# Performance work log

Measured on AMD Instinct MI355X. Metric: run time of the kernel, lower is better.

The kernel has to match this reference:

```python
import jax, jax.numpy as jnp
import numpy as np

B = 2
NUM_EDGES = 50000          # line-graph nodes per sample
N = B * NUM_EDGES          # total nodes in batched graph
E = 400000                 # connectivity edges (before self-loops)
F_IN = 16                  # num_edge_features
TDIM = 64                  # time_embedding_dim
H, C = 4, 32               # heads, hidden_channels
HC = H * C                 # 128
NL_EXTRA = 3               # num_layers - 1
NCLASS = 2
THETA = 1.0
MAX_TIME = 1000.0
NEG_SLOPE = 0.2            # GATv2 leaky_relu slope (PyG default)

def _p(key, shape, s=0.05):
    return jax.random.normal(key, shape, dtype=jnp.float32) * s

def setup_inputs() -> dict:
    key = jax.random.key(0)
    ks = jax.random.split(key, 16)
    return {
        "x": jax.random.normal(ks[0], (N, F_IN), dtype=jnp.float32),
        "edge_index": jax.random.randint(ks[1], (2, E), 0, N, dtype=jnp.int32),
        "t": jax.random.randint(ks[2], (B,), 0, 1000, dtype=jnp.int32),
        "tW0": _p(ks[3], (TDIM, TDIM)), "tb0": jnp.zeros((TDIM,), jnp.float32),
        "tW1": _p(ks[4], (TDIM, TDIM)), "tb1": jnp.zeros((TDIM,), jnp.float32),
        "c0_Wl": _p(ks[5], (F_IN + TDIM, HC)), "c0_bl": jnp.zeros((HC,), jnp.float32),
        "c0_Wr": _p(ks[6], (F_IN + TDIM, HC)), "c0_br": jnp.zeros((HC,), jnp.float32),
        "c0_att": _p(ks[7], (H, C)), "c0_bias": jnp.zeros((HC,), jnp.float32),
        "r0_W": _p(ks[8], (F_IN + TDIM, HC)), "r0_b": jnp.zeros((HC,), jnp.float32),
        "cWl": _p(ks[9], (NL_EXTRA, HC, HC)),
        "cWr": _p(ks[10], (NL_EXTRA, HC, HC)),
        "catt": _p(ks[11], (NL_EXTRA, H, C)),
        "rW": _p(ks[12], (NL_EXTRA, HC, HC)), "rb": jnp.zeros((NL_EXTRA, HC), jnp.float32),
        "fdW": _p(ks[13], (HC, C)), "fdb": jnp.zeros((C,), jnp.float32),
        "acW": _p(ks[14], (C, NCLASS)), "acb": jnp.zeros((NCLASS,), jnp.float32),
    }

def _timestep_embedding(t):
    # Fairseq-style sinusoidal embedding, matches get_timestep_embedding
    ts = t.astype(jnp.float32) * (1000.0 / MAX_TIME)
    half = TDIM // 2
    freqs = jnp.exp(jnp.arange(half, dtype=jnp.float32) * (-jnp.log(10000.0) / (half - 1)))
    ang = ts[:, None] * freqs[None, :]
    return jnp.concatenate([jnp.sin(ang), jnp.cos(ang)], axis=1)  # [B, TDIM]

def _gatv2(x, Wl, bl, Wr, br, att, src, dst):
    # PyG GATv2Conv, concat=True, add_self_loops already in src/dst
    xl = x @ Wl
    xr = x @ Wr
    if bl is not None:
        xl = xl + bl
    if br is not None:
        xr = xr + br
    xl = xl.reshape(N, H, C)
    xr = xr.reshape(N, H, C)
    g = jax.nn.leaky_relu(xl[src] + xr[dst], NEG_SLOPE)          # [Etot, H, C]
    e = jnp.einsum('ehc,hc->eh', g, att)                          # [Etot, H]
    m = jax.ops.segment_max(e, dst, num_segments=N)
    ex = jnp.exp(e - m[dst])
    denom = jax.ops.segment_sum(ex, dst, num_segments=N)
    alpha = ex / denom[dst]
    out = jax.ops.segment_sum(alpha[:, :, None] * xl[src], dst, num_segments=N)
    return out.reshape(N, HC)

def reference(x, edge_index, t, tW0, tb0, tW1, tb1, c0_Wl, c0_bl, c0_Wr, c0_br,
              c0_att, c0_bias, r0_W, r0_b, cWl, cWr, catt, rW, rb,
              fdW, fdb, acW, acb):
    loops = jnp.arange(N, dtype=edge_index.dtype)
    src = jnp.concatenate([edge_index[0], loops])
    dst = jnp.concatenate([edge_index[1], loops])
    te = jax.nn.silu(_timestep_embedding(t) @ tW0 + tb0)
    te = jax.nn.silu(te @ tW1 + tb1)
    te = jnp.repeat(te, NUM_EDGES, axis=0)                        # repeat_interleave
    h = jnp.concatenate([x, te], axis=1)                          # [N, F_IN+TDIM]
    res = jax.nn.relu(h @ r0_W + r0_b)
    h = THETA * jax.nn.relu(_gatv2(h, c0_Wl, c0_bl, c0_Wr, c0_br, c0_att, src, dst) + c0_bias) + res
    for i in range(NL_EXTRA):
        res = jax.nn.relu(h @ rW[i] + rb[i])
        h = THETA * jax.nn.relu(_gatv2(h, cWl[i], None, cWr[i], None, catt[i], src, dst)) + res
    logits = (h @ fdW + fdb) @ acW + acb
    return logits.reshape(B, NUM_EDGES, NCLASS)
```

## Files before the change

kernel.cpp:

```cpp
#include <hip/hip_runtime.h>
#include <stdint.h>

#define NN 100000
#define EE 400000
#define NEDGE 50000
#define NBLK ((NN + 1023) / 1024)

typedef unsigned short u16;
typedef unsigned int u32;
typedef __attribute__((ext_vector_type(8))) __bf16 v8bf;
typedef __attribute__((ext_vector_type(4))) float v4f;

__device__ __forceinline__ float bf2f(u16 u) {
    return (float)__builtin_bit_cast(__bf16, u);
}
__device__ __forceinline__ u16 f2bf(float f) {
    __bf16 b = (__bf16)f;
    return __builtin_bit_cast(u16, b);
}
__device__ __forceinline__ void unpack8(const int4& v, float* f) {
    u32 a = (u32)v.x, b = (u32)v.y, c = (u32)v.z, d = (u32)v.w;
    f[0] = bf2f((u16)(a & 0xffff)); f[1] = bf2f((u16)(a >> 16));
    f[2] = bf2f((u16)(b & 0xffff)); f[3] = bf2f((u16)(b >> 16));
    f[4] = bf2f((u16)(c & 0xffff)); f[5] = bf2f((u16)(c >> 16));
    f[6] = bf2f((u16)(d & 0xffff)); f[7] = bf2f((u16)(d >> 16));
}

struct WPtrs { const float* p[12]; int K[12]; };

__global__ __launch_bounds__(256) void k_setup(WPtrs wp, u16* __restrict__ Wp,
        const int* __restrict__ t,
        const float* __restrict__ tW0, const float* __restrict__ tb0,
        const float* __restrict__ tW1, const float* __restrict__ tb1,
        float* __restrict__ te_out,
        const float* __restrict__ fdW, const float* __restrict__ fdb,
        const float* __restrict__ acW, const float* __restrict__ acb,
        float* __restrict__ Wf, float* __restrict__ bfu,
        const int* __restrict__ ei, int* __restrict__ deg) {
    __shared__ float emb[2][64];
    __shared__ float u1[2][64];
    int b = blockIdx.x, tid = threadIdx.x;
    if (b < 768) {
        int idx = b * 256 + tid;
        int m = idx >> 14;
        int r = idx & 16383;
        int j = r & 7;
        int lane = (r >> 3) & 63;
        int fragid = r >> 9;
        int nt = fragid & 3;
        int ks = (fragid >> 2) & 3;
        int wc = fragid >> 4;
        int k = ks * 32 + ((lane >> 4) << 3) + j;
        int col = wc * 64 + nt * 16 + (lane & 15);
        float f = (k < wp.K[m]) ? wp.p[m][k * 128 + col] : 0.0f;
        Wp[idx] = f2bf(f);
    } else if (b == 768) {
        if (tid < 128) {
            int bb = tid >> 6, j = tid & 63;
            float ts = (float)t[bb];
            int jj = (j < 32) ? j : (j - 32);
            float fr = expf((float)jj * (-logf(10000.0f) / 31.0f));
            float ang = ts * fr;
            emb[bb][j] = (j < 32) ? sinf(ang) : cosf(ang);
        }
        __syncthreads();
        if (tid < 128) {
            int bb = tid >> 6, j = tid & 63;
            float s = tb0[j];
            for (int k = 0; k < 64; ++k) s += emb[bb][k] * tW0[k * 64 + j];
            s = s / (1.0f + expf(-s));
            u1[bb][j] = s;
        }
        __syncthreads();
        if (tid < 128) {
            int bb = tid >> 6, j = tid & 63;
            float s2 = tb1[j];
            for (int k = 0; k < 64; ++k) s2 += u1[bb][k] * tW1[k * 64 + j];
            s2 = s2 / (1.0f + expf(-s2));
            te_out[bb * 64 + j] = s2;
        }
    } else if (b == 769) {
        int r = tid >> 1, c = tid & 1;
        float s = 0.f;
        for (int k = 0; k < 32; ++k) s += fdW[r * 32 + k] * acW[k * 2 + c];
        Wf[tid] = s;
        if (tid < 2) {
            float s2 = acb[tid];
            for (int k = 0; k < 32; ++k) s2 += fdb[k] * acW[k * 2 + tid];
            bfu[tid] = s2;
        }
    } else {
        int e = (b - 770) * 256 + tid;
        if (e < EE) atomicAdd(&deg[ei[EE + e]], 1);
    }
}

__global__ __launch_bounds__(1024) void k_scan1(const int* __restrict__ deg,
                                                int* __restrict__ part, int* __restrict__ bsum) {
    __shared__ int wsum[16], woff[16];
    int tid = threadIdx.x, lane = tid & 63, wid = tid >> 6;
    int idx = blockIdx.x * 1024 + tid;
    int v = (idx < NN) ? deg[idx] : 0;
    int s = v;
#pragma unroll
    for (int off = 1; off < 64; off <<= 1) {
        int tv = __shfl_up(s, off);
        if (lane >= off) s += tv;
    }
    if (lane == 63) wsum[wid] = s;
    __syncthreads();
    if (wid == 0) {
        int ws_ = (lane < 16) ? wsum[lane] : 0;
        int t2 = ws_;
#pragma unroll
        for (int off = 1; off < 16; off <<= 1) {
            int tv = __shfl_up(t2, off);
            if (lane >= off) t2 += tv;
        }
        if (lane < 16) woff[lane] = t2 - ws_;
    }
    __syncthreads();
    int excl = woff[wid] + (s - v);
    if (idx < NN) part[idx] = excl;
    if (tid == 1023) bsum[blockIdx.x] = excl + v;
}

__global__ __launch_bounds__(256) void k_scan3(const int* __restrict__ part, const int* __restrict__ bsum,
                                               int* __restrict__ rowptr, int* __restrict__ cursor) {
    __shared__ int pre[NBLK + 1];
    __shared__ int sh_ws0;
    int tid = threadIdx.x;
    int lane = tid & 63, wid = tid >> 6;
    int v = 0, s = 0;
    if (tid < 128) {
        v = (tid < NBLK) ? bsum[tid] : 0;
        s = v;
#pragma unroll
        for (int off = 1; off < 64; off <<= 1) {
            int tv = __shfl_up(s, off);
            if (lane >= off) s += tv;
        }
        if (tid == 63) sh_ws0 = s;
    }
    __syncthreads();
    if (tid < 128) {
        int excl = (s - v) + (wid ? sh_ws0 : 0);
        if (tid <= NBLK) pre[tid] = excl;
    }
    __syncthreads();
    int idx = blockIdx.x * 256 + tid;
    if (idx > NN) return;
    int val = (idx == NN) ? pre[NBLK] : (part[idx] + pre[idx >> 10]);
    rowptr[idx] = val;
    if (idx < NN) cursor[idx] = val;
}

__global__ __launch_bounds__(256) void k_fill(const int* __restrict__ ei,
                                              int* __restrict__ cursor, int* __restrict__ colv) {
    int e = blockIdx.x * 256 + threadIdx.x;
    if (e >= EE) return;
    int s = ei[e], d = ei[EE + e];
    int pos = atomicAdd(&cursor[d], 1);
    colv[pos] = s;
}

__device__ __forceinline__ void gemm_from_lds(const u16* hT, u16* lTw,
                                              const u16* __restrict__ Wp,
                                              const float* __restrict__ b0,
                                              const float* __restrict__ b1,
                                              const float* __restrict__ b2,
                                              u16* __restrict__ xl, u16* __restrict__ xr,
                                              u16* __restrict__ res,
                                              int lane, int wid, int row0) {
    int wr = wid >> 1, wc = wid & 1;
    const float* bptr[3] = {b0, b1, b2};
    u16* optr[3] = {xl, xr, res};
#pragma unroll
    for (int o = 0; o < 3; ++o) {
        v8bf bF[4][4];
        {
            const u16* wb = Wp + o * 16384 + ((wc * 16) * 64 + lane) * 8;
#pragma unroll
            for (int ks = 0; ks < 4; ++ks)
#pragma unroll
                for (int nt = 0; nt < 4; ++nt)
                    bF[ks][nt] = *reinterpret_cast<const v8bf*>(wb + (ks * 4 + nt) * 512);
        }
        v4f acc[2][4];
        v4f vzero = {0.f, 0.f, 0.f, 0.f};
#pragma unroll
        for (int m = 0; m < 2; ++m)
#pragma unroll
            for (int nt = 0; nt < 4; ++nt) acc[m][nt] = vzero;
#pragma unroll
        for (int ks = 0; ks < 4; ++ks) {
            v8bf aF[2];
#pragma unroll
            for (int m = 0; m < 2; ++m) {
                int row = wr * 32 + m * 16 + (lane & 15);
                int kb = ks * 64 + ((lane >> 4) << 4);
                int sb = kb ^ ((row & 7) << 4);
                aF[m] = *reinterpret_cast<const v8bf*>(reinterpret_cast<const char*>(hT) + row * 256 + sb);
            }
#pragma unroll
            for (int m = 0; m < 2; ++m)
#pragma unroll
                for (int nt = 0; nt < 4; ++nt)
                    acc[m][nt] = __builtin_amdgcn_mfma_f32_16x16x32_bf16(bF[ks][nt], aF[m], acc[m][nt], 0, 0, 0);
        }
        const float* bp = bptr[o];
        u16* op = optr[o];
        int relu = (o == 2);
        float4 bv[4];
#pragma unroll
        for (int nt = 0; nt < 4; ++nt)
            bv[nt] = bp ? *reinterpret_cast<const float4*>(bp + wc * 64 + nt * 16 + ((lane >> 4) << 2))
                        : make_float4(0.f, 0.f, 0.f, 0.f);
#pragma unroll
        for (int p = 0; p < 2; ++p) {
            int rl = lane & 15;
            int cl = (lane >> 4) << 2;
#pragma unroll
            for (int nt = 0; nt < 4; ++nt) {
                float v0 = acc[p][nt][0] + bv[nt].x;
                float v1 = acc[p][nt][1] + bv[nt].y;
                float v2 = acc[p][nt][2] + bv[nt].z;
                float v3 = acc[p][nt][3] + bv[nt].w;
                if (relu) {
                    v0 = fmaxf(v0, 0.f); v1 = fmaxf(v1, 0.f);
                    v2 = fmaxf(v2, 0.f); v3 = fmaxf(v3, 0.f);
                }
                int2 pk;
                pk.x = (int)((u32)f2bf(v0) | ((u32)f2bf(v1) << 16));
                pk.y = (int)((u32)f2bf(v2) | ((u32)f2bf(v3) << 16));
                *reinterpret_cast<int2*>(lTw + rl * 72 + nt * 16 + cl) = pk;
            }
#pragma unroll
            for (int i = 0; i < 2; ++i) {
                int rl2 = i * 8 + (lane >> 3);
                int4 v = *reinterpret_cast<const int4*>(lTw + rl2 * 72 + (lane & 7) * 8);
                int grow = row0 + wr * 32 + p * 16 + rl2;
                if (grow < NN)
                    *reinterpret_cast<int4*>(op + grow * 128 + wc * 64 + (lane & 7) * 8) = v;
            }
        }
    }
}

__global__ __launch_bounds__(256) void k_gemm0(const float* __restrict__ x,
                                               const float* __restrict__ te,
                                               const u16* __restrict__ Wp,
                                               const float* __restrict__ b0,
                                               const float* __restrict__ b1,
                                               const float* __restrict__ b2,
                                               u16* __restrict__ xl, u16* __restrict__ xr,
                                               u16* __restrict__ res) {
    __shared__ __align__(16) u16 lA[64 * 128];
    __shared__ __align__(16) u16 lT[4][16 * 72];
    int tid = threadIdx.x;
    int lane = tid & 63, wid = tid >> 6;
    int row0 = blockIdx.x * 64;

#pragma unroll
    for (int i = 0; i < 4; ++i) {
        int chunk = i * 256 + tid;
        int row = chunk >> 4;
        int c8 = (chunk & 15) << 3;
        int node = row0 + row;
        u32 w_[4];
        if (c8 < 80 && node < NN) {
            const float* sp = (c8 < 16) ? (x + (size_t)node * 16 + c8)
                                        : (te + ((node >= NEDGE) ? 64 : 0) + (c8 - 16));
#pragma unroll
            for (int q = 0; q < 4; ++q)
                w_[q] = (u32)f2bf(sp[2 * q]) | ((u32)f2bf(sp[2 * q + 1]) << 16);
        } else {
            w_[0] = w_[1] = w_[2] = w_[3] = 0;
        }
        int sb = (c8 * 2) ^ ((row & 7) << 4);
        *reinterpret_cast<int4*>(reinterpret_cast<char*>(lA) + row * 256 + sb) =
            make_int4((int)w_[0], (int)w_[1], (int)w_[2], (int)w_[3]);
    }
    __syncthreads();
    gemm_from_lds(lA, lT[wid], Wp, b0, b1, b2, xl, xr, res, lane, wid, row0);
}

__global__ __launch_bounds__(256) void k_gemm3(const u16* __restrict__ A,
                                               const u16* __restrict__ Wp,
                                               const float* __restrict__ b0,
                                               const float* __restrict__ b1,
                                               const float* __restrict__ b2,
                                               u16* __restrict__ xl, u16* __restrict__ xr,
                                               u16* __restrict__ res) {
    __shared__ __align__(16) u16 lA[64 * 128];
    __shared__ __align__(16) u16 lT[4][16 * 72];
    int tid = threadIdx.x;
    int lane = tid & 63, wid = tid >> 6;
    int row0 = blockIdx.x * 64;
#pragma unroll
    for (int i = 0; i < 4; ++i) {
        int chunk = i * 256 + wid * 64 + lane;
        int row = chunk >> 4;
        int cb = (chunk & 15) << 4;
        int scol = cb ^ ((row & 7) << 4);
        const u16* src = A + (size_t)(row0 + row) * 128 + (scol >> 1);
        u16* ldsbase = lA + (size_t)(i * 256 + wid * 64) * 8;
        __builtin_amdgcn_global_load_lds(
            (const __attribute__((address_space(1))) void*)src,
            (__attribute__((address_space(3))) void*)ldsbase, 16, 0, 0);
    }
    __syncthreads();
    gemm_from_lds(lA, lT[wid], Wp, b0, b1, b2, xl, xr, res, lane, wid, row0);
}

__global__ __launch_bounds__(256) void k_gat(const u16* __restrict__ xl, const u16* __restrict__ xr,
                                             const float* __restrict__ att,
                                             const int* __restrict__ rowptr, const int* __restrict__ colv,
                                             const u16* __restrict__ res, const float* __restrict__ bias,
                                             u16* __restrict__ h,
                                             const float* __restrict__ Wf, const float* __restrict__ bfu,
                                             float* __restrict__ out) {
    int tid = threadIdx.x;
    int lane = tid & 63;
    int grp = lane >> 4;
    int s = lane & 15;
    int dst = blockIdx.x * 16 + (tid >> 6) * 4 + grp;
    if (dst >= NN) return;
    int c0 = s * 8;
    float av[8];
    *reinterpret_cast<float4*>(av) = *reinterpret_cast<const float4*>(att + c0);
    *reinterpret_cast<float4*>(av + 4) = *reinterpret_cast<const float4*>(att + c0 + 4);
    int4 xrv = *reinterpret_cast<const int4*>(xr + dst * 128 + c0);
    float xrf[8];
    unpack8(xrv, xrf);
    float den = 0.f;
    float acc[8] = {0.f, 0.f, 0.f, 0.f, 0.f, 0.f, 0.f, 0.f};
    int rbeg = rowptr[dst], rend = rowptr[dst + 1];
    for (int base = rbeg - 1; base < rend; base += 4) {
        int nv = rend - base; if (nv > 4) nv = 4;
        int4 xsv[4];
#pragma unroll
        for (int i = 0; i < 4; ++i) {
            if (i < nv) {
                int r = base + i;
                int src = (r < rbeg) ? dst : colv[r];
                xsv[i] = *reinterpret_cast<const int4*>(xl + (size_t)src * 128 + c0);
            }
        }
#pragma unroll
        for (int i = 0; i < 4; ++i) {
            if (i < nv) {
                float xs[8];
                unpack8(xsv[i], xs);
                float e = 0.f;
#pragma unroll
                for (int j = 0; j < 8; ++j) {
                    float gg = xs[j] + xrf[j];
                    gg = (gg > 0.f) ? gg : 0.2f * gg;
                    e = fmaf(gg, av[j], e);
                }
                e += __shfl_xor(e, 1, 4);
                e += __shfl_xor(e, 2, 4);
                float p = __expf(e);
                den += p;
#pragma unroll
                for (int j = 0; j < 8; ++j) acc[j] = fmaf(p, xs[j], acc[j]);
            }
        }
    }
    float inv = 1.0f / den;
    int4 rv = *reinterpret_cast<const int4*>(res + dst * 128 + c0);
    float rf[8];
    unpack8(rv, rf);
    float bvv[8] = {0.f, 0.f, 0.f, 0.f, 0.f, 0.f, 0.f, 0.f};
    if (bias) {
        *reinterpret_cast<float4*>(bvv) = *reinterpret_cast<const float4*>(bias + c0);
        *reinterpret_cast<float4*>(bvv + 4) = *reinterpret_cast<const float4*>(bias + c0 + 4);
    }
    float of[8];
#pragma unroll
    for (int j = 0; j < 8; ++j)
        of[j] = fmaxf(acc[j] * inv + bvv[j], 0.f) + rf[j];
    if (out) {
        float v0 = 0.f, v1 = 0.f;
#pragma unroll
        for (int j = 0; j < 8; ++j) {
            v0 = fmaf(of[j], Wf[(c0 + j) * 2], v0);
            v1 = fmaf(of[j], Wf[(c0 + j) * 2 + 1], v1);
        }
#pragma unroll
        for (int off = 1; off < 16; off <<= 1) {
            v0 += __shfl_xor(v0, off, 16);
            v1 += __shfl_xor(v1, off, 16);
        }
        if (s == 0) {
            float2 o = make_float2(v0 + bfu[0], v1 + bfu[1]);
            *reinterpret_cast<float2*>(out + dst * 2) = o;
        }
    } else {
        u32 ow[4];
#pragma unroll
        for (int j2 = 0; j2 < 4; ++j2)
            ow[j2] = (u32)f2bf(of[2 * j2]) | ((u32)f2bf(of[2 * j2 + 1]) << 16);
        *reinterpret_cast<int4*>(h + dst * 128 + c0) = make_int4((int)ow[0], (int)ow[1], (int)ow[2], (int)ow[3]);
    }
}

extern "C" void kernel_launch(void* const* d_in, const int* in_sizes, int n_in,
                              void* d_out, int out_size, void* d_ws, size_t ws_size,
                              hipStream_t stream) {
    const float* x      = (const float*)d_in[0];
    const int*   ei     = (const int*)d_in[1];
    const int*   t      = (const int*)d_in[2];
    const float* tW0    = (const float*)d_in[3];
    const float* tb0    = (const float*)d_in[4];
    const float* tW1    = (const float*)d_in[5];
    const float* tb1    = (const float*)d_in[6];
    const float* c0_Wl  = (const float*)d_in[7];
    const float* c0_bl  = (const float*)d_in[8];
    const float* c0_Wr  = (const float*)d_in[9];
    const float* c0_br  = (const float*)d_in[10];
    const float* c0_att = (const float*)d_in[11];
    const float* c0_bias= (const float*)d_in[12];
    const float* r0_W   = (const float*)d_in[13];
    const float* r0_b   = (const float*)d_in[14];
    const float* cWl    = (const float*)d_in[15];
    const float* cWr    = (const float*)d_in[16];
    const float* catt   = (const float*)d_in[17];
    const float* rW     = (const float*)d_in[18];
    const float* rb     = (const float*)d_in[19];
    const float* fdW    = (const float*)d_in[20];
    const float* fdb    = (const float*)d_in[21];
    const float* acW    = (const float*)d_in[22];
    const float* acb    = (const float*)d_in[23];
    (void)in_sizes; (void)n_in; (void)out_size; (void)ws_size;

    char* w = (char*)d_ws;
    const size_t HB = (size_t)NN * 128 * 2;
    float* te   = (float*)w;
    u16* h      = (u16*)(w + 4096);
    u16* xl     = (u16*)(w + 4096 + HB);
    u16* xr     = (u16*)(w + 4096 + 2 * HB);
    u16* res    = (u16*)(w + 4096 + 3 * HB);
    char* p     = w + 4096 + 4 * HB;
    int* deg    = (int*)(p);
    int* rowptr = (int*)(p + (1 << 19));
    int* cursor = (int*)(p + 2 * (1 << 19));
    int* colv   = (int*)(p + 3 * (1 << 19));
    int* part   = (int*)(p + 5 * (1 << 19));
    int* bsum   = (int*)(p + 6 * (1 << 19));
    u16* Wp     = (u16*)(p + 7 * (1 << 19));
    float* Wf   = (float*)(p + 8 * (1 << 19));
    float* bfu  = (float*)(p + 8 * (1 << 19) + 2048);

    WPtrs wp;
    wp.p[0] = c0_Wl; wp.p[1] = c0_Wr; wp.p[2] = r0_W;
    wp.K[0] = 80;    wp.K[1] = 80;    wp.K[2] = 80;
    for (int i = 0; i < 3; ++i) {
        wp.p[3 + 3 * i] = cWl + i * 16384;
        wp.p[4 + 3 * i] = cWr + i * 16384;
        wp.p[5 + 3 * i] = rW + i * 16384;
        wp.K[3 + 3 * i] = 128; wp.K[4 + 3 * i] = 128; wp.K[5 + 3 * i] = 128;
    }

    hipMemsetAsync(deg, 0, NN * sizeof(int), stream);
    k_setup<<<770 + 1563, 256, 0, stream>>>(wp, Wp, t, tW0, tb0, tW1, tb1, te,
                                            fdW, fdb, acW, acb, Wf, bfu, ei, deg);
    k_scan1<<<NBLK, 1024, 0, stream>>>(deg, part, bsum);
    k_scan3<<<(NN + 256) / 256, 256, 0, stream>>>(part, bsum, rowptr, cursor);
    k_fill<<<(EE + 255) / 256, 256, 0, stream>>>(ei, cursor, colv);

    const int GB = (NN + 63) / 64;
    const int GG = (NN + 15) / 16;
    k_gemm0<<<GB, 256, 0, stream>>>(x, te, Wp, c0_bl, c0_br, r0_b, xl, xr, res);
    k_gat<<<GG, 256, 0, stream>>>(xl, xr, c0_att, rowptr, colv, res, c0_bias, h,
                                  nullptr, nullptr, nullptr);
    for (int i = 0; i < 3; ++i) {
        k_gemm3<<<GB, 256, 0, stream>>>(h, Wp + (3 + 3 * i) * 16384, nullptr, nullptr, rb + i * 128, xl, xr, res);
        k_gat<<<GG, 256, 0, stream>>>(xl, xr, catt + i * 128, rowptr, colv, res, nullptr, h,
                                      Wf, bfu, (i == 2) ? (float*)d_out : nullptr);
    }
}
```

Before: 421.8 us.

## Split each destination's edges across four lane groups in GAT aggregation

The GAT aggregation kernel now gives each destination node a full 64-lane wavefront instead of a 16-lane group. The four 16-lane groups take interleaved edge slots and combine their partial softmax denominators and weighted sums with cross-group shuffles. This shortens the serial per-node edge loop and spreads degree imbalance, but it removes the 4-deep batched load unroll, quadruples the grid size and adds reduction shuffles. Only one group writes the output.

```diff
diff --git a/kernel.cpp b/kernel.cpp
--- a/kernel.cpp
+++ b/kernel.cpp
@@ -322,54 +322,49 @@
                                              float* __restrict__ out) {
     int tid = threadIdx.x;
     int lane = tid & 63;
+    int dst = blockIdx.x * 4 + (tid >> 6);
+    if (dst >= NN) return;
     int grp = lane >> 4;
     int s = lane & 15;
-    int dst = blockIdx.x * 16 + (tid >> 6) * 4 + grp;
-    if (dst >= NN) return;
     int c0 = s * 8;
     float av[8];
     *reinterpret_cast<float4*>(av) = *reinterpret_cast<const float4*>(att + c0);
     *reinterpret_cast<float4*>(av + 4) = *reinterpret_cast<const float4*>(att + c0 + 4);
-    int4 xrv = *reinterpret_cast<const int4*>(xr + dst * 128 + c0);
+    int4 xrv = *reinterpret_cast<const int4*>(xr + (size_t)dst * 128 + c0);
     float xrf[8];
     unpack8(xrv, xrf);
     float den = 0.f;
     float acc[8] = {0.f, 0.f, 0.f, 0.f, 0.f, 0.f, 0.f, 0.f};
     int rbeg = rowptr[dst], rend = rowptr[dst + 1];
-    for (int base = rbeg - 1; base < rend; base += 4) {
-        int nv = rend - base; if (nv > 4) nv = 4;
-        int4 xsv[4];
-#pragma unroll
-        for (int i = 0; i < 4; ++i) {
-            if (i < nv) {
-                int r = base + i;
-                int src = (r < rbeg) ? dst : colv[r];
-                xsv[i] = *reinterpret_cast<const int4*>(xl + (size_t)src * 128 + c0);
-            }
-        }
-#pragma unroll
-        for (int i = 0; i < 4; ++i) {
-            if (i < nv) {
-                float xs[8];
-                unpack8(xsv[i], xs);
-                float e = 0.f;
-#pragma unroll
-                for (int j = 0; j < 8; ++j) {
-                    float gg = xs[j] + xrf[j];
-                    gg = (gg > 0.f) ? gg : 0.2f * gg;
-                    e = fmaf(gg, av[j], e);
-                }
-                e += __shfl_xor(e, 1, 4);
-                e += __shfl_xor(e, 2, 4);
-                float p = __expf(e);
-                den += p;
-#pragma unroll
-                for (int j = 0; j < 8; ++j) acc[j] = fmaf(p, xs[j], acc[j]);
-            }
-        }
+    int nslots = rend - rbeg + 1;
+    for (int slot = grp; slot < nslots; slot += 4) {
+        int src = (slot == 0) ? dst : colv[rbeg + slot - 1];
+        int4 xsv = *reinterpret_cast<const int4*>(xl + (size_t)src * 128 + c0);
+        float xs[8];
+        unpack8(xsv, xs);
+        float e = 0.f;
+#pragma unroll
+        for (int j = 0; j < 8; ++j) {
+            float gg = xs[j] + xrf[j];
+            gg = (gg > 0.f) ? gg : 0.2f * gg;
+            e = fmaf(gg, av[j], e);
+        }
+        e += __shfl_xor(e, 1, 4);
+        e += __shfl_xor(e, 2, 4);
+        float p = __expf(e);
+        den += p;
+#pragma unroll
+        for (int j = 0; j < 8; ++j) acc[j] = fmaf(p, xs[j], acc[j]);
+    }
+    den += __shfl_xor(den, 16, 64);
+    den += __shfl_xor(den, 32, 64);
+#pragma unroll
+    for (int j = 0; j < 8; ++j) {
+        acc[j] += __shfl_xor(acc[j], 16, 64);
+        acc[j] += __shfl_xor(acc[j], 32, 64);
     }
     float inv = 1.0f / den;
-    int4 rv = *reinterpret_cast<const int4*>(res + dst * 128 + c0);
+    int4 rv = *reinterpret_cast<const int4*>(res + (size_t)dst * 128 + c0);
     float rf[8];
     unpack8(rv, rf);
     float bvv[8] = {0.f, 0.f, 0.f, 0.f, 0.f, 0.f, 0.f, 0.f};
@@ -393,16 +388,16 @@
             v0 += __shfl_xor(v0, off, 16);
             v1 += __shfl_xor(v1, off, 16);
         }
-        if (s == 0) {
+        if (lane == 0) {
             float2 o = make_float2(v0 + bfu[0], v1 + bfu[1]);
             *reinterpret_cast<float2*>(out + dst * 2) = o;
         }
-    } else {
+    } else if (grp == 0) {
         u32 ow[4];
 #pragma unroll
         for (int j2 = 0; j2 < 4; ++j2)
             ow[j2] = (u32)f2bf(of[2 * j2]) | ((u32)f2bf(of[2 * j2 + 1]) << 16);
-        *reinterpret_cast<int4*>(h + dst * 128 + c0) = make_int4((int)ow[0], (int)ow[1], (int)ow[2], (int)ow[3]);
+        *reinterpret_cast<int4*>(h + (size_t)dst * 128 + c0) = make_int4((int)ow[0], (int)ow[1], (int)ow[2], (int)ow[3]);
     }
 }
 
@@ -471,7 +466,7 @@
     k_fill<<<(EE + 255) / 256, 256, 0, stream>>>(ei, cursor, colv);
 
     const int GB = (NN + 63) / 64;
-    const int GG = (NN + 15) / 16;
+    const int GG = (NN + 3) / 4;
     k_gemm0<<<GB, 256, 0, stream>>>(x, te, Wp, c0_bl, c0_br, r0_b, xl, xr, res);
     k_gat<<<GG, 256, 0, stream>>>(xl, xr, c0_att, rowptr, colv, res, c0_bias, h,
                                   nullptr, nullptr, nullptr);
```

New measurement: 479.5 us. 13.7% more time.
